# Kernel tuning notes

Hardware: AMD Instinct MI355X
Metric: run time of the kernel (lower is better)

## Reference

```python
import jax, jax.numpy as jnp
import numpy as np

B, L, H, D = 64, 2048, 1024, 128  # segments, segment length, hidden, input_dim
N = B * L

def swish(z):
    return z * jax.nn.sigmoid(z)

def setup_inputs() -> dict:
    key = jax.random.key(0)
    ks = jax.random.split(key, 10)
    s = 0.02
    x_seeds = jax.random.normal(ks[0], (N, D), dtype=jnp.float32)
    x_nodes = jax.random.normal(ks[1], (N, D), dtype=jnp.float32)
    W_seed = jax.random.normal(ks[2], (H, D), dtype=jnp.float32) * s
    W_node = jax.random.normal(ks[3], (H, D), dtype=jnp.float32) * s
    W1 = jax.random.normal(ks[4], (H, H), dtype=jnp.float32) * s
    b1 = jnp.zeros((H,), dtype=jnp.float32)
    W2 = jax.random.normal(ks[5], (H, H), dtype=jnp.float32) * s
    b2 = jnp.zeros((H,), dtype=jnp.float32)
    w_ns = jax.random.normal(ks[6], (1, H), dtype=jnp.float32) * s   # node_score_layer (zero-init in src; random for nontrivial baseline)
    W_stop = jax.random.normal(ks[7], (2, H), dtype=jnp.float32) * s  # stopping_score_layer
    starts = jnp.arange(B, dtype=jnp.int32) * L
    indptr = jnp.stack([starts, starts + L, starts + L], axis=1)  # (start, end, candidate_end)
    return {"x_seeds": x_seeds, "x_nodes": x_nodes, "W_seed": W_seed, "W_node": W_node,
            "W1": W1, "b1": b1, "W2": W2, "b2": b2, "w_ns": w_ns, "W_stop": W_stop,
            "indptr": indptr}

def reference(x_seeds, x_nodes, W_seed, W_node, W1, b1, W2, b2, w_ns, W_stop, indptr):
    # embeddings + 2-layer Swish MLP
    h = x_seeds @ W_seed.T + x_nodes @ W_node.T            # [N, H]
    h = swish(h @ W1.T + b1)
    h = swish(h @ W2.T + b2)
    node_scores = (h @ w_ns.T)[:, 0]                       # [N]
    # ragged segments (uniform length L) defined by indptr starts
    nb = indptr.shape[0]
    seg_len = h.shape[0] // nb                             # static L
    idx = indptr[:, 0][:, None] + jnp.arange(seg_len)      # [B, L]
    h_seg = h[idx]                                         # [B, L, H]
    stop_node = h_seg.mean(axis=1)                         # [B, H] per-segment mean pool
    node_logits = jax.nn.log_softmax(node_scores[idx], axis=1)          # [B, L]
    stop_logits = jax.nn.log_softmax(stop_node @ W_stop.T, axis=1)      # [B, 2]
    # concat([node_logits + stop0, stop1]) per segment
    return jnp.concatenate([node_logits + stop_logits[:, :1], stop_logits[:, 1:]], axis=1)  # [B, L+1]
```

## Files before the change

kernel.cpp:

```cpp
#include <hip/hip_runtime.h>

typedef float f32x4 __attribute__((ext_vector_type(4)));
typedef __bf16 bf16x8 __attribute__((ext_vector_type(8)));
typedef unsigned short u16x8 __attribute__((ext_vector_type(8)));

#define DEVINL static __device__ __forceinline__

DEVINL unsigned short f2bf(float f) {
    unsigned int u = __builtin_bit_cast(unsigned int, f);
    u += 0x7fffu + ((u >> 16) & 1u);
    return (unsigned short)(u >> 16);
}
DEVINL float bf2f(unsigned short u) {
    unsigned int x = ((unsigned int)u) << 16;
    return __builtin_bit_cast(float, x);
}

#define GLD16(gp, lp)                                                          \
    __builtin_amdgcn_global_load_lds(                                          \
        (const __attribute__((address_space(1))) void*)(gp),                   \
        (__attribute__((address_space(3))) void*)(lp), 16, 0, 0)

__global__ void pack_cat_k(const float* __restrict__ s0, const float* __restrict__ s1,
                           unsigned short* __restrict__ dst, int nchunks) {
    int e = blockIdx.x * 256 + threadIdx.x;
    if (e >= nchunks) return;
    int row = e >> 5, ch = e & 31;
    const float* src = (ch < 16) ? (s0 + (size_t)row * 128 + ch * 8)
                                 : (s1 + (size_t)row * 128 + (ch - 16) * 8);
    float4 a = *(const float4*)src;
    float4 b = *(const float4*)(src + 4);
    u16x8 o;
    o[0] = f2bf(a.x); o[1] = f2bf(a.y); o[2] = f2bf(a.z); o[3] = f2bf(a.w);
    o[4] = f2bf(b.x); o[5] = f2bf(b.y); o[6] = f2bf(b.z); o[7] = f2bf(b.w);
    *(u16x8*)(dst + (size_t)e * 8) = o;
}

__global__ void cvt_k(const float* __restrict__ s, unsigned short* __restrict__ d, int nchunks) {
    int e = blockIdx.x * 256 + threadIdx.x;
    if (e >= nchunks) return;
    float4 a = *(const float4*)(s + (size_t)e * 8);
    float4 b = *(const float4*)(s + (size_t)e * 8 + 4);
    u16x8 o;
    o[0] = f2bf(a.x); o[1] = f2bf(a.y); o[2] = f2bf(a.z); o[3] = f2bf(a.w);
    o[4] = f2bf(b.x); o[5] = f2bf(b.y); o[6] = f2bf(b.z); o[7] = f2bf(b.w);
    *(u16x8*)(d + (size_t)e * 8) = o;
}

__global__ void gemm1_k(const float* __restrict__ xs, const float* __restrict__ xn,
                        const unsigned short* __restrict__ B,
                        unsigned short* __restrict__ C, int M, int N) {
    __shared__ unsigned short As[128 * 32];
    __shared__ unsigned short Bs[128 * 32];
    const int tid  = threadIdx.x;
    const int lane = tid & 63;
    const int wv   = tid >> 6;
    const int wr   = wv >> 1, wc = wv & 1;
    const int ntn  = N >> 7;

    const int nwg = gridDim.x;
    const int xcd = blockIdx.x & 7, blk = blockIdx.x >> 3;
    const int q = nwg >> 3, rr = nwg & 7;
    const int logical = (xcd < rr ? xcd * (q + 1) : rr * (q + 1) + (xcd - rr) * q) + blk;

    const int im   = logical / ntn, in = logical % ntn;
    const size_t rowA0 = (size_t)im * 128, rowB0 = (size_t)in * 128;

    const int e0 = tid, e1 = tid + 256;
    const int ra0 = e0 >> 2, ca0 = (e0 & 3) * 8;
    const int ra1 = e1 >> 2, ca1 = (e1 & 3) * 8;

    f32x4 acc[4][4] = {};
    const int frow = lane & 15;
    const int kb   = (lane >> 4) * 8;

    for (int k0 = 0; k0 < 256; k0 += 32) {
        GLD16(B + (rowB0 + ra0) * 256 + k0 + ca0, (char*)Bs + e0 * 16);
        GLD16(B + (rowB0 + ra1) * 256 + k0 + ca1, (char*)Bs + e1 * 16);
        const float* src = (k0 < 128) ? xs : xn;
        const int kk = k0 & 127;
        {
            const float* p = src + (rowA0 + ra0) * 128 + kk + ca0;
            float4 a = *(const float4*)p, b = *(const float4*)(p + 4);
            u16x8 o;
            o[0] = f2bf(a.x); o[1] = f2bf(a.y); o[2] = f2bf(a.z); o[3] = f2bf(a.w);
            o[4] = f2bf(b.x); o[5] = f2bf(b.y); o[6] = f2bf(b.z); o[7] = f2bf(b.w);
            *(u16x8*)((char*)As + e0 * 16) = o;
        }
        {
            const float* p = src + (rowA0 + ra1) * 128 + kk + ca1;
            float4 a = *(const float4*)p, b = *(const float4*)(p + 4);
            u16x8 o;
            o[0] = f2bf(a.x); o[1] = f2bf(a.y); o[2] = f2bf(a.z); o[3] = f2bf(a.w);
            o[4] = f2bf(b.x); o[5] = f2bf(b.y); o[6] = f2bf(b.z); o[7] = f2bf(b.w);
            *(u16x8*)((char*)As + e1 * 16) = o;
        }
        __syncthreads();

        bf16x8 af[4], bfr[4];
#pragma unroll
        for (int m = 0; m < 4; ++m)
            af[m] = *(const bf16x8*)&As[(wr * 64 + m * 16 + frow) * 32 + kb];
#pragma unroll
        for (int n = 0; n < 4; ++n)
            bfr[n] = *(const bf16x8*)&Bs[(wc * 64 + n * 16 + frow) * 32 + kb];
#pragma unroll
        for (int m = 0; m < 4; ++m)
#pragma unroll
            for (int n = 0; n < 4; ++n)
                acc[m][n] = __builtin_amdgcn_mfma_f32_16x16x32_bf16(af[m], bfr[n], acc[m][n], 0, 0, 0);
        __syncthreads();
    }

    const int r4 = (lane >> 4) * 4;
    const int cc = lane & 15;
#pragma unroll
    for (int n = 0; n < 4; ++n) {
        const int col = (int)rowB0 + wc * 64 + n * 16 + cc;
#pragma unroll
        for (int m = 0; m < 4; ++m) {
            const size_t row = rowA0 + wr * 64 + m * 16 + r4;
#pragma unroll
            for (int r = 0; r < 4; ++r)
                C[(row + r) * (size_t)N + col] = f2bf(acc[m][n][r]);
        }
    }
}

template <int EPI>
__global__ void gemm_bt_k(const unsigned short* __restrict__ A,
                          const unsigned short* __restrict__ B,
                          const float* __restrict__ bias,
                          unsigned short* __restrict__ C,
                          const float* __restrict__ wns,
                          float* __restrict__ sc,
                          float* __restrict__ pl,
                          int M, int N, int K) {
    __shared__ unsigned short As[128 * 32];
    __shared__ unsigned short Bs[128 * 32];
    const int tid  = threadIdx.x;
    const int lane = tid & 63;
    const int wv   = tid >> 6;
    const int wr   = wv >> 1, wc = wv & 1;
    const int ntn  = N >> 7;

    const int nwg = gridDim.x;
    const int xcd = blockIdx.x & 7, blk = blockIdx.x >> 3;
    const int q = nwg >> 3, rr = nwg & 7;
    const int logical = (xcd < rr ? xcd * (q + 1) : rr * (q + 1) + (xcd - rr) * q) + blk;

    const int im   = logical / ntn, in = logical % ntn;
    const size_t rowA0 = (size_t)im * 128, rowB0 = (size_t)in * 128;

    const int e0 = tid, e1 = tid + 256;
    const int ra0 = e0 >> 2, ca0 = (e0 & 3) * 8;
    const int ra1 = e1 >> 2, ca1 = (e1 & 3) * 8;

    f32x4 acc[4][4] = {};
    const int frow = lane & 15;
    const int kb   = (lane >> 4) * 8;

    for (int k0 = 0; k0 < K; k0 += 32) {
        GLD16(A + (rowA0 + ra0) * K + k0 + ca0, (char*)As + e0 * 16);
        GLD16(A + (rowA0 + ra1) * K + k0 + ca1, (char*)As + e1 * 16);
        GLD16(B + (rowB0 + ra0) * K + k0 + ca0, (char*)Bs + e0 * 16);
        GLD16(B + (rowB0 + ra1) * K + k0 + ca1, (char*)Bs + e1 * 16);
        __syncthreads();

        bf16x8 af[4], bfr[4];
#pragma unroll
        for (int m = 0; m < 4; ++m)
            af[m] = *(const bf16x8*)&As[(wr * 64 + m * 16 + frow) * 32 + kb];
#pragma unroll
        for (int n = 0; n < 4; ++n)
            bfr[n] = *(const bf16x8*)&Bs[(wc * 64 + n * 16 + frow) * 32 + kb];
#pragma unroll
        for (int m = 0; m < 4; ++m)
#pragma unroll
            for (int n = 0; n < 4; ++n)
                acc[m][n] = __builtin_amdgcn_mfma_f32_16x16x32_bf16(af[m], bfr[n], acc[m][n], 0, 0, 0);
        __syncthreads();
    }

    const int r4 = (lane >> 4) * 4;
    const int cc = lane & 15;

    if (EPI == 2) {
#pragma unroll
        for (int n = 0; n < 4; ++n) {
            const float bv = bias[(int)rowB0 + wc * 64 + n * 16 + cc];
#pragma unroll
            for (int m = 0; m < 4; ++m)
#pragma unroll
                for (int r = 0; r < 4; ++r) {
                    float v = acc[m][n][r] + bv;
                    acc[m][n][r] = v / (1.0f + __expf(-v));
                }
        }
#pragma unroll
        for (int m = 0; m < 4; ++m)
#pragma unroll
            for (int r = 0; r < 4; ++r) {
                float s = 0.f;
#pragma unroll
                for (int n = 0; n < 4; ++n)
                    s += acc[m][n][r] * wns[(int)rowB0 + wc * 64 + n * 16 + cc];
#pragma unroll
                for (int o = 1; o < 16; o <<= 1) s += __shfl_xor(s, o);
                if (cc == 0)
                    atomicAdd(&sc[rowA0 + wr * 64 + m * 16 + r4 + r], s);
            }
        const int seg = (int)(rowA0 >> 11);
#pragma unroll
        for (int n = 0; n < 4; ++n) {
            float p = 0.f;
#pragma unroll
            for (int m = 0; m < 4; ++m)
#pragma unroll
                for (int r = 0; r < 4; ++r) p += acc[m][n][r];
            p += __shfl_xor(p, 16);
            p += __shfl_xor(p, 32);
            if ((lane >> 4) == 0)
                atomicAdd(&pl[seg * 1024 + (int)rowB0 + wc * 64 + n * 16 + cc],
                          p * (1.0f / 2048.0f));
        }
        return;
    }

#pragma unroll
    for (int n = 0; n < 4; ++n) {
        const int col = (int)rowB0 + wc * 64 + n * 16 + cc;
        const float bv = bias[col];
#pragma unroll
        for (int m = 0; m < 4; ++m) {
            const size_t row = rowA0 + wr * 64 + m * 16 + r4;
#pragma unroll
            for (int r = 0; r < 4; ++r) {
                float v = acc[m][n][r] + bv;
                v = v / (1.0f + __expf(-v));
                C[(row + r) * (size_t)N + col] = f2bf(v);
            }
        }
    }
}

__global__ void stop_k(const float* __restrict__ pool, const float* __restrict__ Wstop,
                       float* __restrict__ stp, float* __restrict__ out) {
    const int b = blockIdx.x, t = threadIdx.x;
    float a0 = 0.f, a1 = 0.f;
#pragma unroll
    for (int j = 0; j < 4; ++j) {
        const int hcol = t + j * 256;
        const float pv = pool[b * 1024 + hcol];
        a0 += pv * Wstop[hcol];
        a1 += pv * Wstop[1024 + hcol];
    }
    const int lane = t & 63, wv = t >> 6;
#pragma unroll
    for (int off = 32; off; off >>= 1) { a0 += __shfl_down(a0, off); a1 += __shfl_down(a1, off); }
    __shared__ float r0[4], r1[4];
    if (lane == 0) { r0[wv] = a0; r1[wv] = a1; }
    __syncthreads();
    if (t == 0) {
        const float s0 = r0[0] + r0[1] + r0[2] + r0[3];
        const float s1 = r1[0] + r1[1] + r1[2] + r1[3];
        const float m  = fmaxf(s0, s1);
        const float lse = m + __logf(__expf(s0 - m) + __expf(s1 - m));
        stp[b * 2] = s0 - lse;
        out[(size_t)b * 2049 + 2048] = s1 - lse;
    }
}

__global__ void node_k(const float* __restrict__ sc, const float* __restrict__ stp,
                       float* __restrict__ out) {
    const int b = blockIdx.x, t = threadIdx.x;
    const float* s = sc + (size_t)b * 2048;
    float v[8];
    float mx = -3.4e38f;
#pragma unroll
    for (int j = 0; j < 8; ++j) { v[j] = s[t + j * 256]; mx = fmaxf(mx, v[j]); }
    const int lane = t & 63, wv = t >> 6;
    __shared__ float red[4];
#pragma unroll
    for (int off = 32; off; off >>= 1) mx = fmaxf(mx, __shfl_down(mx, off));
    if (lane == 0) red[wv] = mx;
    __syncthreads();
    mx = fmaxf(fmaxf(red[0], red[1]), fmaxf(red[2], red[3]));
    float se = 0.f;
#pragma unroll
    for (int j = 0; j < 8; ++j) se += __expf(v[j] - mx);
    __syncthreads();
#pragma unroll
    for (int off = 32; off; off >>= 1) se += __shfl_down(se, off);
    if (lane == 0) red[wv] = se;
    __syncthreads();
    se = red[0] + red[1] + red[2] + red[3];
    const float base = stp[b * 2] - mx - __logf(se);
#pragma unroll
    for (int j = 0; j < 8; ++j) out[(size_t)b * 2049 + t + j * 256] = v[j] + base;
}

extern "C" void kernel_launch(void* const* d_in, const int* in_sizes, int n_in,
                              void* d_out, int out_size, void* d_ws, size_t ws_size,
                              hipStream_t stream) {
    (void)in_sizes; (void)n_in; (void)out_size;
    const float* x_seeds = (const float*)d_in[0];
    const float* x_nodes = (const float*)d_in[1];
    const float* W_seed  = (const float*)d_in[2];
    const float* W_node  = (const float*)d_in[3];
    const float* W1      = (const float*)d_in[4];
    const float* b1      = (const float*)d_in[5];
    const float* W2      = (const float*)d_in[6];
    const float* b2      = (const float*)d_in[7];
    const float* w_ns    = (const float*)d_in[8];
    const float* W_stop  = (const float*)d_in[9];
    float* out = (float*)d_out;

    const int N = 131072, H = 1024, B = 64;

    char* ws = (char*)d_ws;
    size_t off = 0;
    auto alloc = [&](size_t bytes) {
        char* p = ws + off;
        off += (bytes + 255) & ~(size_t)255;
        return p;
    };
    unsigned short* wcat = (unsigned short*)alloc((size_t)H * 256 * 2);
    unsigned short* W1b  = (unsigned short*)alloc((size_t)H * H * 2);
    unsigned short* W2b  = (unsigned short*)alloc((size_t)H * H * 2);
    float* scores = (float*)alloc((size_t)N * 4);
    float* pool   = (float*)alloc((size_t)B * H * 4);
    float* stp    = (float*)alloc((size_t)B * 2 * 4);

    const size_t per_row = 1024 * 2 + 1024 * 2;
    size_t avail = (ws_size > off + (1u << 20)) ? (ws_size - off - (1u << 20)) : 0;
    long long mc_ll = (long long)(avail / per_row) / 2048 * 2048;
    int Mc = (int)(mc_ll < 2048 ? 2048 : (mc_ll > 65536 ? 65536 : mc_ll));

    unsigned short* h0_c = (unsigned short*)alloc((size_t)Mc * H * 2);
    unsigned short* h1_c = (unsigned short*)alloc((size_t)Mc * H * 2);

    hipMemsetAsync(pool, 0, (size_t)B * H * 4, stream);
    hipMemsetAsync(scores, 0, (size_t)N * 4, stream);

    pack_cat_k<<<(H * 32) / 256, 256, 0, stream>>>(W_seed, W_node, wcat, H * 32);
    cvt_k<<<(H * H / 8) / 256, 256, 0, stream>>>(W1, W1b, H * H / 8);
    cvt_k<<<(H * H / 8) / 256, 256, 0, stream>>>(W2, W2b, H * H / 8);

    for (int base = 0; base < N; base += Mc) {
        const int m = (N - base < Mc) ? (N - base) : Mc;
        const int grid128 = (m / 128) * (H / 128);
        gemm1_k<<<grid128, 256, 0, stream>>>(x_seeds + (size_t)base * 128,
                                             x_nodes + (size_t)base * 128,
                                             wcat, h0_c, m, H);
        gemm_bt_k<1><<<grid128, 256, 0, stream>>>(h0_c, W1b, b1, h1_c,
                                                  nullptr, nullptr, nullptr, m, H, H);
        gemm_bt_k<2><<<grid128, 256, 0, stream>>>(h1_c, W2b, b2, nullptr,
                                                  w_ns, scores + base,
                                                  pool + (size_t)(base / 2048) * H, m, H, H);
    }

    stop_k<<<B, 256, 0, stream>>>(pool, W_stop, stp, out);
    node_k<<<B, 256, 0, stream>>>(scores, stp, out);
}
```

Before: 1.086 ms.

## Add K=64 swizzled-LDS GEMM with XCD-aware block remap for layer one

Adds a new bf16 MFMA GEMM kernel for the first MLP layer. Each K step loads a 128x64 tile into LDS with an XOR swizzle to avoid bank conflicts, and blocks are remapped so neighbouring tiles land on the same XCD for better L2 reuse. It also raises the chunk-size cap from 65536 rows to the full N, so fewer chunked launches are needed when the workspace allows. The new kernel has no software pipelining, since it synchronises after every load, and the second layer still uses the old kernel.

```diff
diff --git a/kernel.cpp b/kernel.cpp
--- a/kernel.cpp
+++ b/kernel.cpp
@@ -244,6 +244,92 @@
     }
 }
 
+DEVINL int swzK(int b) { return b ^ (((b >> 7) & 7) << 4); }
+
+template <int EPI>
+__global__ void gemm_bt64_k(const unsigned short* __restrict__ A,
+                            const unsigned short* __restrict__ B,
+                            const float* __restrict__ bias,
+                            unsigned short* __restrict__ C,
+                            int M, int N, int K) {
+    __shared__ unsigned short As[128 * 64];
+    __shared__ unsigned short Bs[128 * 64];
+    const int tid  = threadIdx.x;
+    const int lane = tid & 63;
+    const int wv   = tid >> 6;
+    const int wr   = wv >> 1, wc = wv & 1;
+    const int ntn  = N >> 7;
+
+    const int nwg = gridDim.x;
+    const int xcd = blockIdx.x & 7, blk = blockIdx.x >> 3;
+    const int q = nwg >> 3, rr = nwg & 7;
+    const int logical = (xcd < rr ? xcd * (q + 1) : rr * (q + 1) + (xcd - rr) * q) + blk;
+
+    const int im   = logical / ntn, in = logical % ntn;
+    const size_t rowA0 = (size_t)im * 128, rowB0 = (size_t)in * 128;
+
+    f32x4 acc[4][4] = {};
+    const int frow = lane & 15;
+    const int q16  = (lane >> 4) * 16;
+
+    for (int k0 = 0; k0 < K; k0 += 64) {
+#pragma unroll
+        for (int j = 0; j < 4; ++j) {
+            const int c = tid + j * 256;
+            const int row = c >> 3;
+            const int gc = (c & 7) ^ (row & 7);
+            GLD16(A + (rowA0 + row) * K + k0 + gc * 8, (char*)As + c * 16);
+        }
+#pragma unroll
+        for (int j = 0; j < 4; ++j) {
+            const int c = tid + j * 256;
+            const int row = c >> 3;
+            const int gc = (c & 7) ^ (row & 7);
+            GLD16(B + (rowB0 + row) * K + k0 + gc * 8, (char*)Bs + c * 16);
+        }
+        __syncthreads();
+
+#pragma unroll
+        for (int kh = 0; kh < 2; ++kh) {
+            bf16x8 af[4], bfr[4];
+#pragma unroll
+            for (int m = 0; m < 4; ++m) {
+                const int b = (wr * 64 + m * 16 + frow) * 128 + kh * 64 + q16;
+                af[m] = *(const bf16x8*)((char*)As + swzK(b));
+            }
+#pragma unroll
+            for (int n = 0; n < 4; ++n) {
+                const int b = (wc * 64 + n * 16 + frow) * 128 + kh * 64 + q16;
+                bfr[n] = *(const bf16x8*)((char*)Bs + swzK(b));
+            }
+#pragma unroll
+            for (int m = 0; m < 4; ++m)
+#pragma unroll
+                for (int n = 0; n < 4; ++n)
+                    acc[m][n] = __builtin_amdgcn_mfma_f32_16x16x32_bf16(af[m], bfr[n], acc[m][n], 0, 0, 0);
+        }
+        __syncthreads();
+    }
+
+    const int r4 = (lane >> 4) * 4;
+    const int cc = lane & 15;
+#pragma unroll
+    for (int n = 0; n < 4; ++n) {
+        const int col = (int)rowB0 + wc * 64 + n * 16 + cc;
+        const float bv = bias[col];
+#pragma unroll
+        for (int m = 0; m < 4; ++m) {
+            const size_t row = rowA0 + wr * 64 + m * 16 + r4;
+#pragma unroll
+            for (int r = 0; r < 4; ++r) {
+                float v = acc[m][n][r] + bv;
+                if (EPI == 1) v = v / (1.0f + __expf(-v));
+                C[(row + r) * (size_t)N + col] = f2bf(v);
+            }
+        }
+    }
+}
+
 __global__ void stop_k(const float* __restrict__ pool, const float* __restrict__ Wstop,
                        float* __restrict__ stp, float* __restrict__ out) {
     const int b = blockIdx.x, t = threadIdx.x;
@@ -335,7 +421,7 @@
     const size_t per_row = 1024 * 2 + 1024 * 2;
     size_t avail = (ws_size > off + (1u << 20)) ? (ws_size - off - (1u << 20)) : 0;
     long long mc_ll = (long long)(avail / per_row) / 2048 * 2048;
-    int Mc = (int)(mc_ll < 2048 ? 2048 : (mc_ll > 65536 ? 65536 : mc_ll));
+    int Mc = (int)(mc_ll < 2048 ? 2048 : (mc_ll > N ? N : mc_ll));
 
     unsigned short* h0_c = (unsigned short*)alloc((size_t)Mc * H * 2);
     unsigned short* h1_c = (unsigned short*)alloc((size_t)Mc * H * 2);
@@ -353,8 +439,7 @@
         gemm1_k<<<grid128, 256, 0, stream>>>(x_seeds + (size_t)base * 128,
                                              x_nodes + (size_t)base * 128,
                                              wcat, h0_c, m, H);
-        gemm_bt_k<1><<<grid128, 256, 0, stream>>>(h0_c, W1b, b1, h1_c,
-                                                  nullptr, nullptr, nullptr, m, H, H);
+        gemm_bt64_k<1><<<grid128, 256, 0, stream>>>(h0_c, W1b, b1, h1_c, m, H, H);
         gemm_bt_k<2><<<grid128, 256, 0, stream>>>(h1_c, W2b, b2, nullptr,
                                                   w_ns, scores + base,
                                                   pool + (size_t)(base / 2048) * H, m, H, H);
```

Measured after the change: 1.038 ms. 4.4% less time.
